# Kernel optimization log

Measured on AMD Instinct MI355X. Metric: run time of the kernel, lower is better.

Reference implementation:

```python
import jax, jax.numpy as jnp
import numpy as np

D_MODEL, D_K, D_V = 1024, 64, 64
B, S = 4, 2048

def setup_inputs() -> dict:
    key = jax.random.key(0)
    ks = jax.random.split(key, 9)
    lim = 1.0 / np.sqrt(D_MODEL)
    return {
        "query": jax.random.normal(ks[0], (B, S, D_MODEL), jnp.float32),
        "key":   jax.random.normal(ks[1], (B, S, D_MODEL), jnp.float32),
        "value": jax.random.normal(ks[2], (B, S, D_MODEL), jnp.float32),
        "Wq": jax.random.uniform(ks[3], (D_MODEL, D_K), jnp.float32, -lim, lim),
        "bq": jax.random.uniform(ks[4], (D_K,), jnp.float32, -lim, lim),
        "Wk": jax.random.uniform(ks[5], (D_MODEL, D_K), jnp.float32, -lim, lim),
        "bk": jax.random.uniform(ks[6], (D_K,), jnp.float32, -lim, lim),
        "Wv": jax.random.uniform(ks[7], (D_MODEL, D_V), jnp.float32, -lim, lim),
        "bv": jax.random.uniform(ks[8], (D_V,), jnp.float32, -lim, lim),
    }

def reference(query, key, value, Wq, bq, Wk, bk, Wv, bv):
    # Linear projections: [B,S,d_model] -> [B,S,d_k/d_v]
    q = jnp.einsum("bsd,dk->bsk", query, Wq) + bq
    k = jnp.einsum("bsd,dk->bsk", key, Wk) + bk
    v = jnp.einsum("bsd,dv->bsv", value, Wv) + bv
    scale = 1.0 / jnp.sqrt(jnp.asarray(q.shape[-1], q.dtype))
    scores = jnp.einsum("bqk,bsk->bqs", q, k) * scale  # [B,S,S]
    attn = jax.nn.softmax(scores, axis=-1)
    return jnp.einsum("bqs,bsv->bqv", attn, v)  # [B,S,d_v]
```

## Files before the change

kernel.cpp:

```cpp
#include <hip/hip_runtime.h>
#include <hip/hip_bf16.h>


typedef __attribute__((ext_vector_type(8))) short bf16x8;
typedef __attribute__((ext_vector_type(4))) float f32x4;

#define MFMA16(a, b, c) __builtin_amdgcn_mfma_f32_16x16x32_bf16((a), (b), (c), 0, 0, 0)

__device__ __forceinline__ unsigned short f2bf(float x) {
    unsigned int u = __float_as_uint(x);
    u = (u + 0x7FFFu + ((u >> 16) & 1u)) >> 16;
    return (unsigned short)u;
}

__global__ __launch_bounds__(256) void prep_w(
    const float* __restrict__ Wq, const float* __restrict__ Wk,
    const float* __restrict__ Wv, unsigned short* __restrict__ Wt) {
    int idx = blockIdx.x * 256 + threadIdx.x;
    int t = idx >> 16;
    int r = idx & 0xFFFF;
    int n = r >> 10, kk = r & 1023;
    const float* W = (t == 0) ? Wq : ((t == 1) ? Wk : Wv);
    Wt[idx] = f2bf(W[kk * 64 + n]);
}

__global__ __launch_bounds__(256) void proj_kernel(
    const float* __restrict__ xq, const float* __restrict__ xk,
    const float* __restrict__ xv, const unsigned short* __restrict__ Wt,
    const float* __restrict__ bq, const float* __restrict__ bk,
    const float* __restrict__ bv, unsigned short* __restrict__ outq,
    unsigned short* __restrict__ outk, unsigned short* __restrict__ outvt) {
    const int chunk = blockIdx.x;
    const int t = chunk >> 8;
    const int rb = chunk & 255;
    const int row0 = rb * 32;
    const float* __restrict__ x = (t == 0) ? xq : ((t == 1) ? xk : xv);
    const float* __restrict__ bias = (t == 0) ? bq : ((t == 1) ? bk : bv);
    const unsigned short* __restrict__ Wtt = Wt + t * 65536;

    __shared__ __align__(16) unsigned short xl[32][72];
    __shared__ __align__(16) unsigned short wl[64][72];

    const int tid = threadIdx.x;
    const int w = tid >> 6, l = tid & 63;
    const int lo = l & 15, q4 = l >> 4;
    const int rowt = (w & 1) * 16;
    const int colb = (w >> 1) * 32;

    const int lr = tid >> 3;
    const int lkc = (tid & 7) * 8;
    const int wr = tid >> 2;
    const int wkc = (tid & 3) * 16;

    f32x4 acc[2];
    for (int i = 0; i < 2; i++)
        for (int j = 0; j < 4; j++) acc[i][j] = 0.f;

    const float* xrow = x + (size_t)(row0 + lr) * 1024 + lkc;
    const unsigned short* wrow = Wtt + (size_t)wr * 1024 + wkc;

    float4 px0 = *(const float4*)(xrow);
    float4 px1 = *(const float4*)(xrow + 4);
    int4 pw0 = *(const int4*)(wrow);
    int4 pw1 = *(const int4*)(wrow + 8);

    for (int s = 0; s < 16; ++s) {
        __syncthreads();
        {
            int4 d;
            d.x = f2bf(px0.x) | ((int)f2bf(px0.y) << 16);
            d.y = f2bf(px0.z) | ((int)f2bf(px0.w) << 16);
            d.z = f2bf(px1.x) | ((int)f2bf(px1.y) << 16);
            d.w = f2bf(px1.z) | ((int)f2bf(px1.w) << 16);
            *(int4*)&xl[lr][lkc] = d;
            *(int4*)&wl[wr][wkc] = pw0;
            *(int4*)&wl[wr][wkc + 8] = pw1;
        }
        __syncthreads();
        if (s < 15) {
            const float* xn = xrow + (s + 1) * 64;
            px0 = *(const float4*)(xn);
            px1 = *(const float4*)(xn + 4);
            const unsigned short* wn = wrow + (s + 1) * 64;
            pw0 = *(const int4*)(wn);
            pw1 = *(const int4*)(wn + 8);
        }
        bf16x8 a0 = *(const bf16x8*)&xl[rowt + lo][q4 * 8];
        bf16x8 a1 = *(const bf16x8*)&xl[rowt + lo][32 + q4 * 8];
#pragma unroll
        for (int ci = 0; ci < 2; ++ci) {
            bf16x8 b0 = *(const bf16x8*)&wl[colb + ci * 16 + lo][q4 * 8];
            bf16x8 b1 = *(const bf16x8*)&wl[colb + ci * 16 + lo][32 + q4 * 8];
            acc[ci] = MFMA16(a0, b0, acc[ci]);
            acc[ci] = MFMA16(a1, b1, acc[ci]);
        }
    }
#pragma unroll
    for (int ci = 0; ci < 2; ++ci) {
        float bb = bias[colb + ci * 16 + lo];
#pragma unroll
        for (int i = 0; i < 4; i++) acc[ci][i] += bb;
    }
    if (t == 0) {
        const float SC = 0.125f * 1.44269504088896340736f;
#pragma unroll
        for (int ci = 0; ci < 2; ++ci)
#pragma unroll
            for (int i = 0; i < 4; i++) acc[ci][i] *= SC;
    }
    if (t < 2) {
        unsigned short* out = (t == 0) ? outq : outk;
#pragma unroll
        for (int ci = 0; ci < 2; ++ci)
#pragma unroll
            for (int i = 0; i < 4; i++)
                out[(size_t)(row0 + rowt + q4 * 4 + i) * 64 + colb + ci * 16 + lo] =
                    f2bf(acc[ci][i]);
    } else {
        int b = row0 >> 11;
        int sl = (row0 & 2047) + rowt + q4 * 4;
#pragma unroll
        for (int ci = 0; ci < 2; ++ci) {
            int vf = colb + ci * 16 + lo;
            ushort4 h;
            h.x = f2bf(acc[ci][0]);
            h.y = f2bf(acc[ci][1]);
            h.z = f2bf(acc[ci][2]);
            h.w = f2bf(acc[ci][3]);
            *(ushort4*)&outvt[(size_t)(b * 64 + vf) * 2048 + sl] = h;
        }
    }
}

__global__ __launch_bounds__(256) void flash_kernel(
    const unsigned short* __restrict__ q, const unsigned short* __restrict__ k,
    const unsigned short* __restrict__ vt, float* __restrict__ Opart,
    float* __restrict__ lpart) {
    const int bx = blockIdx.x;
    const int xcd = bx & 7;
    const int b = xcd >> 1;
    const int j = ((bx >> 3) << 1) | (xcd & 1);
    const int ks = j & 3;
    const int qb = j >> 2;
    const int w = threadIdx.x >> 6, l = threadIdx.x & 63;
    const int lo = l & 15, q4 = l >> 4;

    __shared__ __align__(16) unsigned short pl[4][16][72];

    const int srow = qb * 64 + w * 16;

    const unsigned short* qp = q + (size_t)(b * 2048 + srow + lo) * 64 + q4 * 8;
    bf16x8 aq0 = *(const bf16x8*)(qp);
    bf16x8 aq1 = *(const bf16x8*)(qp + 32);

    f32x4 O[4];
    for (int i = 0; i < 4; i++)
        for (int j2 = 0; j2 < 4; j2++) O[i][j2] = 0.f;
    float ll[4] = {0.f, 0.f, 0.f, 0.f};

    for (int kt = 0; kt < 8; ++kt) {
        const int kb = ks * 512 + kt * 64;
        f32x4 S[4];
        for (int i = 0; i < 4; i++)
            for (int j2 = 0; j2 < 4; j2++) S[i][j2] = 0.f;
        const unsigned short* kp = k + (size_t)(b * 2048 + kb + lo) * 64 + q4 * 8;
#pragma unroll
        for (int ct = 0; ct < 4; ++ct) {
            bf16x8 b0 = *(const bf16x8*)(kp + ct * 1024);
            bf16x8 b1 = *(const bf16x8*)(kp + ct * 1024 + 32);
            S[ct] = MFMA16(aq0, b0, S[ct]);
            S[ct] = MFMA16(aq1, b1, S[ct]);
        }
#pragma unroll
        for (int i = 0; i < 4; i++) {
#pragma unroll
            for (int ct = 0; ct < 4; ++ct) {
                float p = exp2f(S[ct][i]);
                S[ct][i] = p;
                ll[i] += p;
            }
#pragma unroll
            for (int ct = 0; ct < 4; ++ct)
                pl[w][q4 * 4 + i][ct * 16 + lo] = f2bf(S[ct][i]);
        }
        bf16x8 ap0 = *(const bf16x8*)&pl[w][lo][q4 * 8];
        bf16x8 ap1 = *(const bf16x8*)&pl[w][lo][32 + q4 * 8];
        const unsigned short* vp =
            vt + (size_t)(b * 64 + lo) * 2048 + kb + q4 * 8;
#pragma unroll
        for (int ct = 0; ct < 4; ++ct) {
            bf16x8 v0 = *(const bf16x8*)(vp + (size_t)ct * 16 * 2048);
            bf16x8 v1 = *(const bf16x8*)(vp + (size_t)ct * 16 * 2048 + 32);
            O[ct] = MFMA16(ap0, v0, O[ct]);
            O[ct] = MFMA16(ap1, v1, O[ct]);
        }
    }
    float* op = Opart + ((size_t)(b * 4 + ks) * 2048 + srow) * 64;
#pragma unroll
    for (int ct = 0; ct < 4; ++ct)
#pragma unroll
        for (int i = 0; i < 4; i++)
            op[(size_t)(q4 * 4 + i) * 64 + ct * 16 + lo] = O[ct][i];
#pragma unroll
    for (int i = 0; i < 4; i++) {
        float s = ll[i];
        s += __shfl_xor(s, 1);
        s += __shfl_xor(s, 2);
        s += __shfl_xor(s, 4);
        s += __shfl_xor(s, 8);
        if (lo == 0)
            lpart[(size_t)(b * 4 + ks) * 2048 + srow + q4 * 4 + i] = s;
    }
}

__global__ __launch_bounds__(256) void combine_kernel(
    const float* __restrict__ Opart, const float* __restrict__ lpart,
    float* __restrict__ out) {
    int idx = blockIdx.x * 256 + threadIdx.x;
    int rowi = idx >> 4;
    int v4 = (idx & 15) * 4;
    int b = rowi >> 11, s = rowi & 2047;
    float L = 0.f;
#pragma unroll
    for (int ks = 0; ks < 4; ++ks)
        L += lpart[(size_t)(b * 4 + ks) * 2048 + s];
    float inv = 1.f / L;
    float ax = 0.f, ay = 0.f, az = 0.f, aw = 0.f;
#pragma unroll
    for (int ks = 0; ks < 4; ++ks) {
        const float4 o =
            *(const float4*)&Opart[((size_t)(b * 4 + ks) * 2048 + s) * 64 + v4];
        ax += o.x;
        ay += o.y;
        az += o.z;
        aw += o.w;
    }
    float4 res = make_float4(ax * inv, ay * inv, az * inv, aw * inv);
    *(float4*)&out[(size_t)rowi * 64 + v4] = res;
}

extern "C" void kernel_launch(void* const* d_in, const int* in_sizes, int n_in,
                              void* d_out, int out_size, void* d_ws,
                              size_t ws_size, hipStream_t stream) {
    const float* xq = (const float*)d_in[0];
    const float* xk = (const float*)d_in[1];
    const float* xv = (const float*)d_in[2];
    const float* Wq = (const float*)d_in[3];
    const float* bq = (const float*)d_in[4];
    const float* Wk = (const float*)d_in[5];
    const float* bk = (const float*)d_in[6];
    const float* Wv = (const float*)d_in[7];
    const float* bv = (const float*)d_in[8];
    float* out = (float*)d_out;

    char* ws = (char*)d_ws;
    unsigned short* qb = (unsigned short*)(ws);
    unsigned short* kb = (unsigned short*)(ws + (1u << 20));
    unsigned short* vtb = (unsigned short*)(ws + (2u << 20));
    unsigned short* Wt = (unsigned short*)(ws + (3u << 20));
    float* Opart = (float*)(ws + 3538944);
    float* lpart = (float*)(ws + 11927552);

    hipLaunchKernelGGL(prep_w, dim3(768), dim3(256), 0, stream, Wq, Wk, Wv, Wt);
    hipLaunchKernelGGL(proj_kernel, dim3(768), dim3(256), 0, stream, xq, xk, xv,
                       Wt, bq, bk, bv, qb, kb, vtb);
    hipLaunchKernelGGL(flash_kernel, dim3(512), dim3(256), 0, stream, qb, kb,
                       vtb, Opart, lpart);
    hipLaunchKernelGGL(combine_kernel, dim3(512), dim3(256), 0, stream, Opart,
                       lpart, out);
}
```

Measured before the change: 174.4 us.

## Rewrite projection kernel to load MFMA fragments directly from global memory

The projection kernel no longer stages x and W tiles through shared memory with per-step barriers. Each of two waves now owns 16 rows and all 64 output columns, loads its x fragment straight from global memory, converts it to bf16 in registers, and reads W fragments from global (L2-cached) memory for four MFMAs per k-step. The V transpose goes through a small per-wave LDS buffer. This removes the barriers and LDS traffic, at the cost of uncoalesced strided global loads and redundant W reads per wave.

```diff
diff --git a/kernel.cpp b/kernel.cpp
--- a/kernel.cpp
+++ b/kernel.cpp
@@ -11,6 +11,9 @@
     unsigned int u = __float_as_uint(x);
     u = (u + 0x7FFFu + ((u >> 16) & 1u)) >> 16;
     return (unsigned short)u;
+}
+__device__ __forceinline__ int pk2(float a, float b) {
+    return (int)f2bf(a) | ((int)f2bf(b) << 16);
 }
 
 __global__ __launch_bounds__(256) void prep_w(
@@ -24,7 +27,7 @@
     Wt[idx] = f2bf(W[kk * 64 + n]);
 }
 
-__global__ __launch_bounds__(256) void proj_kernel(
+__global__ __launch_bounds__(128) void proj_kernel(
     const float* __restrict__ xq, const float* __restrict__ xk,
     const float* __restrict__ xv, const unsigned short* __restrict__ Wt,
     const float* __restrict__ bq, const float* __restrict__ bk,
@@ -33,101 +36,76 @@
     const int chunk = blockIdx.x;
     const int t = chunk >> 8;
     const int rb = chunk & 255;
-    const int row0 = rb * 32;
     const float* __restrict__ x = (t == 0) ? xq : ((t == 1) ? xk : xv);
     const float* __restrict__ bias = (t == 0) ? bq : ((t == 1) ? bk : bv);
     const unsigned short* __restrict__ Wtt = Wt + t * 65536;
 
-    __shared__ __align__(16) unsigned short xl[32][72];
-    __shared__ __align__(16) unsigned short wl[64][72];
-
-    const int tid = threadIdx.x;
-    const int w = tid >> 6, l = tid & 63;
+    const int w = threadIdx.x >> 6, l = threadIdx.x & 63;
     const int lo = l & 15, q4 = l >> 4;
-    const int rowt = (w & 1) * 16;
-    const int colb = (w >> 1) * 32;
-
-    const int lr = tid >> 3;
-    const int lkc = (tid & 7) * 8;
-    const int wr = tid >> 2;
-    const int wkc = (tid & 3) * 16;
-
-    f32x4 acc[2];
-    for (int i = 0; i < 2; i++)
-        for (int j = 0; j < 4; j++) acc[i][j] = 0.f;
-
-    const float* xrow = x + (size_t)(row0 + lr) * 1024 + lkc;
-    const unsigned short* wrow = Wtt + (size_t)wr * 1024 + wkc;
-
-    float4 px0 = *(const float4*)(xrow);
-    float4 px1 = *(const float4*)(xrow + 4);
-    int4 pw0 = *(const int4*)(wrow);
-    int4 pw1 = *(const int4*)(wrow + 8);
-
-    for (int s = 0; s < 16; ++s) {
-        __syncthreads();
-        {
-            int4 d;
-            d.x = f2bf(px0.x) | ((int)f2bf(px0.y) << 16);
-            d.y = f2bf(px0.z) | ((int)f2bf(px0.w) << 16);
-            d.z = f2bf(px1.x) | ((int)f2bf(px1.y) << 16);
-            d.w = f2bf(px1.z) | ((int)f2bf(px1.w) << 16);
-            *(int4*)&xl[lr][lkc] = d;
-            *(int4*)&wl[wr][wkc] = pw0;
-            *(int4*)&wl[wr][wkc + 8] = pw1;
-        }
-        __syncthreads();
-        if (s < 15) {
-            const float* xn = xrow + (s + 1) * 64;
-            px0 = *(const float4*)(xn);
-            px1 = *(const float4*)(xn + 4);
-            const unsigned short* wn = wrow + (s + 1) * 64;
-            pw0 = *(const int4*)(wn);
-            pw1 = *(const int4*)(wn + 8);
-        }
-        bf16x8 a0 = *(const bf16x8*)&xl[rowt + lo][q4 * 8];
-        bf16x8 a1 = *(const bf16x8*)&xl[rowt + lo][32 + q4 * 8];
-#pragma unroll
-        for (int ci = 0; ci < 2; ++ci) {
-            bf16x8 b0 = *(const bf16x8*)&wl[colb + ci * 16 + lo][q4 * 8];
-            bf16x8 b1 = *(const bf16x8*)&wl[colb + ci * 16 + lo][32 + q4 * 8];
-            acc[ci] = MFMA16(a0, b0, acc[ci]);
-            acc[ci] = MFMA16(a1, b1, acc[ci]);
-        }
-    }
-#pragma unroll
-    for (int ci = 0; ci < 2; ++ci) {
-        float bb = bias[colb + ci * 16 + lo];
-#pragma unroll
-        for (int i = 0; i < 4; i++) acc[ci][i] += bb;
-    }
-    if (t == 0) {
-        const float SC = 0.125f * 1.44269504088896340736f;
-#pragma unroll
-        for (int ci = 0; ci < 2; ++ci)
-#pragma unroll
-            for (int i = 0; i < 4; i++) acc[ci][i] *= SC;
-    }
+    const int row0 = rb * 32 + w * 16;
+
+    __shared__ __align__(16) unsigned short plv[2][16][24];
+
+    const float* xb = x + (size_t)(row0 + lo) * 1024 + q4 * 8;
+    const unsigned short* wb = Wtt + (size_t)lo * 1024 + q4 * 8;
+
+    f32x4 acc[4];
+#pragma unroll
+    for (int ci = 0; ci < 4; ci++)
+        for (int i = 0; i < 4; i++) acc[ci][i] = 0.f;
+
+    for (int ks = 0; ks < 32; ++ks) {
+        const int k0 = ks * 32;
+        float4 xa = *(const float4*)(xb + k0);
+        float4 xc = *(const float4*)(xb + k0 + 4);
+        int4 bi;
+        bi.x = pk2(xa.x, xa.y);
+        bi.y = pk2(xa.z, xa.w);
+        bi.z = pk2(xc.x, xc.y);
+        bi.w = pk2(xc.z, xc.w);
+        bf16x8 bfrag = *(bf16x8*)&bi;
+#pragma unroll
+        for (int ci = 0; ci < 4; ++ci) {
+            bf16x8 afrag = *(const bf16x8*)(wb + ci * 16384 + k0);
+            acc[ci] = MFMA16(afrag, bfrag, acc[ci]);
+        }
+    }
+
+    const float SCQ = 0.125f * 1.44269504088896340736f;
+#pragma unroll
+    for (int ci = 0; ci < 4; ++ci) {
+        const float4 bb = *(const float4*)&bias[ci * 16 + q4 * 4];
+        acc[ci][0] += bb.x;
+        acc[ci][1] += bb.y;
+        acc[ci][2] += bb.z;
+        acc[ci][3] += bb.w;
+        if (t == 0)
+#pragma unroll
+            for (int i = 0; i < 4; i++) acc[ci][i] *= SCQ;
+    }
+
     if (t < 2) {
         unsigned short* out = (t == 0) ? outq : outk;
 #pragma unroll
-        for (int ci = 0; ci < 2; ++ci)
-#pragma unroll
-            for (int i = 0; i < 4; i++)
-                out[(size_t)(row0 + rowt + q4 * 4 + i) * 64 + colb + ci * 16 + lo] =
-                    f2bf(acc[ci][i]);
-    } else {
-        int b = row0 >> 11;
-        int sl = (row0 & 2047) + rowt + q4 * 4;
-#pragma unroll
-        for (int ci = 0; ci < 2; ++ci) {
-            int vf = colb + ci * 16 + lo;
+        for (int ci = 0; ci < 4; ++ci) {
             ushort4 h;
             h.x = f2bf(acc[ci][0]);
             h.y = f2bf(acc[ci][1]);
             h.z = f2bf(acc[ci][2]);
             h.w = f2bf(acc[ci][3]);
-            *(ushort4*)&outvt[(size_t)(b * 64 + vf) * 2048 + sl] = h;
+            *(ushort4*)&out[(size_t)(row0 + lo) * 64 + ci * 16 + q4 * 4] = h;
+        }
+    } else {
+        const int b = row0 >> 11;
+        const int sl = row0 & 2047;
+#pragma unroll
+        for (int ci = 0; ci < 4; ++ci) {
+#pragma unroll
+            for (int i = 0; i < 4; i++)
+                plv[w][q4 * 4 + i][lo] = f2bf(acc[ci][i]);
+            ushort4 hh = *(ushort4*)&plv[w][l & 15][(l >> 4) * 4];
+            *(ushort4*)&outvt[(size_t)(b * 64 + ci * 16 + (l & 15)) * 2048 +
+                              sl + (l >> 4) * 4] = hh;
         }
     }
 }
@@ -262,7 +240,7 @@
     float* lpart = (float*)(ws + 11927552);
 
     hipLaunchKernelGGL(prep_w, dim3(768), dim3(256), 0, stream, Wq, Wk, Wv, Wt);
-    hipLaunchKernelGGL(proj_kernel, dim3(768), dim3(256), 0, stream, xq, xk, xv,
+    hipLaunchKernelGGL(proj_kernel, dim3(768), dim3(128), 0, stream, xq, xk, xv,
                        Wt, bq, bk, bv, qb, kb, vtb);
     hipLaunchKernelGGL(flash_kernel, dim3(512), dim3(256), 0, stream, qb, kb,
                        vtb, Opart, lpart);
```

Result: slower. 186.8 us (+7.1%).
